# Kernel optimization log

Hardware: AMD Instinct MI355X
Metric: run time of the kernel (lower is better)

The kernel has to match this reference:

```python
import jax, jax.numpy as jnp
import numpy as np

B, N, D, F = 4096, 64, 64, 4096
KP_DIM = N * (N + 1) // 2  # 2080
# static row-major triu/tril index lists (matches torch.masked_select ordering)
_TRIU_I, _TRIU_J = (np.array(a) for a in np.triu_indices(N, 0))
_TRIL_I, _TRIL_J = (np.array(a) for a in np.tril_indices(N, 0))


def setup_inputs() -> dict:
    key = jax.random.key(0)
    k1, k2, k3, k4 = jax.random.split(key, 4)
    feature_emb = jax.random.normal(k1, (B, N, D), dtype=jnp.float32)
    # xavier_normal for [D, D]
    std = float(np.sqrt(2.0 / (D + D)))
    kp_W = jax.random.normal(k2, (D, D), dtype=jnp.float32) * std
    # nn.Linear weights are [out_features, in_features]
    bound = float(1.0 / np.sqrt(KP_DIM))
    W_triu = jax.random.uniform(k3, (F, KP_DIM), dtype=jnp.float32, minval=-bound, maxval=bound)
    W_tril = jax.random.uniform(k4, (F, KP_DIM), dtype=jnp.float32, minval=-bound, maxval=bound)
    return {"feature_emb": feature_emb, "kp_W": kp_W, "W_triu": W_triu, "W_tril": W_tril}


def reference(feature_emb, kp_W, W_triu, W_tril):
    # embs_kp[b,i,j] = e[b,i,:] @ kp_W @ e[b,j,:]  -> [B, N, N]
    embs_kp = jnp.einsum("bnd,de,bme->bnm", feature_emb, kp_W, feature_emb)
    triu = embs_kp[:, _TRIU_I, _TRIU_J]  # [B, kp_dim], row-major order
    tril = embs_kp[:, _TRIL_I, _TRIL_J]  # [B, kp_dim]
    embs_flatten = feature_emb.reshape(feature_emb.shape[0], -1)  # [B, N*D]
    view_1 = triu @ W_triu.T  # [B, F]
    view_2 = tril @ W_tril.T  # [B, F]
    return (embs_flatten, view_1, view_2)
```

## Files before the change

kernel.cpp:

```cpp
#include <hip/hip_runtime.h>

typedef __bf16 bf16x8 __attribute__((ext_vector_type(8)));
typedef float f32x4 __attribute__((ext_vector_type(4)));
typedef unsigned short u16x4 __attribute__((ext_vector_type(4)));
typedef unsigned short u16x8 __attribute__((ext_vector_type(8)));

#define KP 2112
#define NT 33

__device__ __forceinline__ unsigned short f2bf(float f) {
  unsigned int u = __builtin_bit_cast(unsigned int, f);
  u += 0x7FFFu + ((u >> 16) & 1u);
  return (unsigned short)(u >> 16);
}

__device__ __forceinline__ bf16x8 ld_frag(const unsigned short* p) {
  return __builtin_bit_cast(bf16x8, *(const u16x8*)p);
}

#define MFMA16(a, b, c) __builtin_amdgcn_mfma_f32_16x16x32_bf16((a), (b), (c), 0, 0, 0)

__device__ __forceinline__ void cp16(const void* g, void* l) {
  __builtin_amdgcn_global_load_lds(
      (const __attribute__((address_space(1))) unsigned int*)g,
      (__attribute__((address_space(3))) unsigned int*)l, 16, 0, 0);
}

__device__ __forceinline__ void barrier_sync() {
  asm volatile("" ::: "memory");
  __builtin_amdgcn_s_barrier();
  __builtin_amdgcn_sched_barrier(0);
}

#define VMWAIT(N) asm volatile("s_waitcnt vmcnt(" #N ")" ::: "memory")

__global__ __launch_bounds__(256) void cvt_pad(const float* __restrict__ in,
                                               unsigned short* __restrict__ out) {
  const int total = 4096 * (KP / 4);
  int i = blockIdx.x * 256 + threadIdx.x;
  const int stride = gridDim.x * 256;
  for (; i < total; i += stride) {
    const int row = i / (KP / 4);
    const int c4 = i - row * (KP / 4);
    u16x4 o = {0, 0, 0, 0};
    if (c4 < 520) {
      float4 v = *(const float4*)(in + (size_t)row * 2080 + c4 * 4);
      o[0] = f2bf(v.x); o[1] = f2bf(v.y); o[2] = f2bf(v.z); o[3] = f2bf(v.w);
    }
    ((u16x4*)out)[i] = o;
  }
}

__global__ __launch_bounds__(256) void prep_wt(const float* __restrict__ W,
                                               unsigned short* __restrict__ Wt) {
  const int tid = threadIdx.x;
#pragma unroll
  for (int j = 0; j < 16; ++j) {
    const int o = tid * 16 + j;
    const int c = o >> 6, d = o & 63;
    Wt[o] = f2bf(W[d * 64 + c]);
  }
}

__global__ __launch_bounds__(256) void batch_kp(
    const float* __restrict__ E,
    const unsigned short* __restrict__ Wt,
    float* __restrict__ out0,
    unsigned short* __restrict__ triu,
    unsigned short* __restrict__ tril)
{
  __shared__ __align__(16) unsigned short sE[64 * 64];
  __shared__ __align__(16) unsigned short sWt[64 * 64];
  __shared__ __align__(16) unsigned short sT[64 * 64];

  const int b = blockIdx.x;
  const int tid = threadIdx.x;
  const float* Eb = E + (size_t)b * 4096;
  float* o0 = out0 + (size_t)b * 4096;

  cp16(Wt + tid * 8, sWt + tid * 8);
  cp16(Wt + 2048 + tid * 8, sWt + 2048 + tid * 8);

#pragma unroll
  for (int it = 0; it < 4; ++it) {
    const int flat = it * 1024 + tid * 4;
    float4 v = *(const float4*)(Eb + flat);
    *(float4*)(o0 + flat) = v;
    u16x4 e;
    e[0] = f2bf(v.x); e[1] = f2bf(v.y); e[2] = f2bf(v.z); e[3] = f2bf(v.w);
    *(u16x4*)(sE + flat) = e;
  }
  __syncthreads();

  const int lane = tid & 63, w = tid >> 6;
  const int fr = lane & 15;
  const int fk = (lane >> 4) << 3;
  const int qr = (lane >> 4) << 2;

#pragma unroll
  for (int ct = 0; ct < 4; ++ct) {
    f32x4 acc = {0.f, 0.f, 0.f, 0.f};
#pragma unroll
    for (int k2 = 0; k2 < 2; ++k2) {
      bf16x8 a = ld_frag(sE + (w * 16 + fr) * 64 + k2 * 32 + fk);
      bf16x8 bb = ld_frag(sWt + (ct * 16 + fr) * 64 + k2 * 32 + fk);
      acc = MFMA16(a, bb, acc);
    }
#pragma unroll
    for (int r = 0; r < 4; ++r)
      sT[(w * 16 + qr + r) * 64 + ct * 16 + fr] = f2bf(acc[r]);
  }
  __syncthreads();

  unsigned short* tu = triu + (size_t)b * KP;
  unsigned short* tl = tril + (size_t)b * KP;
  if (tid < 32) { tu[2080 + tid] = 0; tl[2080 + tid] = 0; }
#pragma unroll
  for (int ct = 0; ct < 4; ++ct) {
    f32x4 acc = {0.f, 0.f, 0.f, 0.f};
#pragma unroll
    for (int k2 = 0; k2 < 2; ++k2) {
      bf16x8 a = ld_frag(sT + (w * 16 + fr) * 64 + k2 * 32 + fk);
      bf16x8 bb = ld_frag(sE + (ct * 16 + fr) * 64 + k2 * 32 + fk);
      acc = MFMA16(a, bb, acc);
    }
#pragma unroll
    for (int r = 0; r < 4; ++r) {
      const int i = w * 16 + qr + r;
      const int j = ct * 16 + fr;
      const unsigned short v = f2bf(acc[r]);
      if (j >= i) tu[i * 64 - ((i * (i - 1)) >> 1) + (j - i)] = v;
      if (j <= i) tl[((i * (i + 1)) >> 1) + j] = v;
    }
  }
}

__global__ __launch_bounds__(512, 2) void gemm_views(
    const unsigned short* __restrict__ triu, const unsigned short* __restrict__ tril,
    const unsigned short* __restrict__ Wu, const unsigned short* __restrict__ Wl,
    float* __restrict__ dout)
{
  __shared__ __align__(16) unsigned short lds[65536];

  const int z = blockIdx.z;
  const unsigned short* Ag = z ? tril : triu;
  const unsigned short* Bg = z ? Wl : Wu;
  float* C = dout + (size_t)16777216 * (size_t)(1 + z);

  const int tid = threadIdx.x;
  const int lane = tid & 63, wv = tid >> 6;
  const int m0 = blockIdx.y << 8, n0 = blockIdx.x << 8;

  const int lr = lane >> 3;
  const int cuch = (lane & 7) ^ lr;
  const int rA = wv * 8 + lr;
  const int rB = (wv & 3) * 8 + (wv >> 2) * 64 + lr;
  const unsigned short* gA = Ag + (size_t)(m0 + rA) * KP + cuch * 8;
  const unsigned short* gB = Bg + (size_t)(n0 + rB) * KP + cuch * 8;
  const int dA = tid * 8;
  const int dB = (wv & 3) * 512 + (wv >> 2) * 4096 + lane * 8;

  const int fr = lane & 15, fq = lane >> 4;
  const int sx0 = ((fq ^ (fr & 7))) * 8;
  const int sx1 = (((4 + fq) ^ (fr & 7))) * 8;
  const int rowA0 = (wv >> 2) * 128 + fr;
  const int rowB0 = (wv & 3) * 64 + fr;

  f32x4 acc[8][4] = {};
  bf16x8 af0[4], af1[4], bh0[2], bh1[2];

#define STAGE_A(B_, KT, OFF) do { \
    cp16(gA + (size_t)(OFF) * KP + (KT) * 64, lds + (B_) * 32768 + (OFF) * 64 + dA); \
    cp16(gA + (size_t)((OFF) + 128) * KP + (KT) * 64, \
         lds + (B_) * 32768 + ((OFF) + 128) * 64 + dA); \
  } while (0)
#define STAGE_B(B_, KT, OFF) do { \
    cp16(gB + (size_t)(OFF) * KP + (KT) * 64, \
         lds + (B_) * 32768 + 16384 + (OFF) * 64 + dB); \
    cp16(gB + (size_t)((OFF) + 128) * KP + (KT) * 64, \
         lds + (B_) * 32768 + 16384 + ((OFF) + 128) * 64 + dB); \
  } while (0)

#define PHASE(B_, MH, NH, LA, LB, STAGE_STMT, WAIT_STMT) do { \
    if (LA) { \
      const unsigned short* pa = lds + (B_) * 32768 + ((rowA0 + (MH) * 64) << 6); \
      _Pragma("unroll") for (int mt = 0; mt < 4; ++mt) { \
        af0[mt] = ld_frag(pa + mt * 1024 + sx0); \
        af1[mt] = ld_frag(pa + mt * 1024 + sx1); } } \
    if (LB) { \
      const unsigned short* pb = lds + (B_) * 32768 + 16384 + ((rowB0 + (NH) * 32) << 6); \
      _Pragma("unroll") for (int nt = 0; nt < 2; ++nt) { \
        bh0[nt] = ld_frag(pb + nt * 1024 + sx0); \
        bh1[nt] = ld_frag(pb + nt * 1024 + sx1); } } \
    STAGE_STMT; \
    barrier_sync(); \
    __builtin_amdgcn_s_setprio(1); \
    _Pragma("unroll") for (int mt = 0; mt < 4; ++mt) \
    _Pragma("unroll") for (int nt = 0; nt < 2; ++nt) { \
      acc[(MH)*4+mt][(NH)*2+nt] = MFMA16(af0[mt], bh0[nt], acc[(MH)*4+mt][(NH)*2+nt]); \
      acc[(MH)*4+mt][(NH)*2+nt] = MFMA16(af1[mt], bh1[nt], acc[(MH)*4+mt][(NH)*2+nt]); } \
    __builtin_amdgcn_s_setprio(0); \
    WAIT_STMT; \
    barrier_sync(); \
  } while (0)

  STAGE_A(0, 0, 0);
  STAGE_B(0, 0, 0);
  STAGE_A(0, 0, 64);
  STAGE_B(0, 0, 32);
  VMWAIT(4);
  barrier_sync();

  for (int t = 0; t < NT - 1; ++t) {
    const int cb = t & 1, nb = cb ^ 1, nk = t + 1;
    PHASE(cb, 0, 0, 1, 1, STAGE_A(nb, nk, 0),  VMWAIT(4));
    PHASE(cb, 1, 0, 1, 0, STAGE_B(nb, nk, 0),  VMWAIT(4));
    PHASE(cb, 1, 1, 0, 1, STAGE_A(nb, nk, 64), (void)0);
    PHASE(cb, 0, 1, 1, 0, STAGE_B(nb, nk, 32), VMWAIT(4));
  }
  {
    const int cb = (NT - 1) & 1;
    PHASE(cb, 0, 0, 1, 1, (void)0, VMWAIT(2));
    PHASE(cb, 1, 0, 1, 0, (void)0, VMWAIT(0));
    PHASE(cb, 1, 1, 0, 1, (void)0, (void)0);
    PHASE(cb, 0, 1, 1, 0, (void)0, (void)0);
  }

  const int qr = fq << 2;
  const int crow = m0 + (wv >> 2) * 128 + qr;
  const int ccol = n0 + (wv & 3) * 64 + fr;
#pragma unroll
  for (int mt = 0; mt < 8; ++mt)
#pragma unroll
    for (int nt = 0; nt < 4; ++nt) {
      float* cp = C + (size_t)(crow + mt * 16) * 4096 + (ccol + nt * 16);
#pragma unroll
      for (int r = 0; r < 4; ++r) cp[(size_t)r * 4096] = acc[mt][nt][r];
    }
#undef STAGE_A
#undef STAGE_B
#undef PHASE
}

extern "C" void kernel_launch(void* const* d_in, const int* in_sizes, int n_in,
                              void* d_out, int out_size, void* d_ws, size_t ws_size,
                              hipStream_t stream) {
  const float* feat  = (const float*)d_in[0];
  const float* kpW   = (const float*)d_in[1];
  const float* Wtriu = (const float*)d_in[2];
  const float* Wtril = (const float*)d_in[3];
  float* out = (float*)d_out;

  const size_t per = (size_t)4096 * KP;
  unsigned short* triu_bf = (unsigned short*)d_ws;
  unsigned short* tril_bf = triu_bf + per;
  unsigned short* Wu_bf   = tril_bf + per;
  unsigned short* Wl_bf   = Wu_bf + per;
  unsigned short* Wt_bf   = Wl_bf + per;

  cvt_pad<<<dim3(1024), dim3(256), 0, stream>>>(Wtriu, Wu_bf);
  cvt_pad<<<dim3(1024), dim3(256), 0, stream>>>(Wtril, Wl_bf);
  prep_wt<<<dim3(1), dim3(256), 0, stream>>>(kpW, Wt_bf);
  batch_kp<<<dim3(4096), dim3(256), 0, stream>>>(feat, Wt_bf, out, triu_bf, tril_bf);
  gemm_views<<<dim3(16, 16, 2), dim3(512), 0, stream>>>(triu_bf, tril_bf, Wu_bf, Wl_bf, out);
}
```

Before: 429.1 us.

## Restructure GEMM main loop into k-half phases with deeper prefetch schedule

Reorganizes the bf16 MFMA GEMM main loop so each phase covers one K-half with four N-tiles, rather than two K-halves with two N-tiles. LDS fragment loads for the next phase are issued before the current MFMAs, and global-to-LDS staging now runs up to two k-tiles ahead, overwriting regions of the current buffer once they are consumed. The aim is better overlap of LDS reads and global loads with MFMA work. In exchange it uses more fragment registers, and its hand-counted vmcnt waits, barrier placement and buffer reuse are fragile enough to risk races.

```diff
diff --git a/kernel.cpp b/kernel.cpp
--- a/kernel.cpp
+++ b/kernel.cpp
@@ -161,13 +161,11 @@
   const int dB = (wv & 3) * 512 + (wv >> 2) * 4096 + lane * 8;
 
   const int fr = lane & 15, fq = lane >> 4;
-  const int sx0 = ((fq ^ (fr & 7))) * 8;
-  const int sx1 = (((4 + fq) ^ (fr & 7))) * 8;
   const int rowA0 = (wv >> 2) * 128 + fr;
   const int rowB0 = (wv & 3) * 64 + fr;
 
   f32x4 acc[8][4] = {};
-  bf16x8 af0[4], af1[4], bh0[2], bh1[2];
+  bf16x8 aA_[4], aB_[4], bA_[4], bB_[4];
 
 #define STAGE_A(B_, KT, OFF) do { \
     cp16(gA + (size_t)(OFF) * KP + (KT) * 64, lds + (B_) * 32768 + (OFF) * 64 + dA); \
@@ -180,50 +178,64 @@
     cp16(gB + (size_t)((OFF) + 128) * KP + (KT) * 64, \
          lds + (B_) * 32768 + 16384 + ((OFF) + 128) * 64 + dB); \
   } while (0)
-
-#define PHASE(B_, MH, NH, LA, LB, STAGE_STMT, WAIT_STMT) do { \
-    if (LA) { \
-      const unsigned short* pa = lds + (B_) * 32768 + ((rowA0 + (MH) * 64) << 6); \
-      _Pragma("unroll") for (int mt = 0; mt < 4; ++mt) { \
-        af0[mt] = ld_frag(pa + mt * 1024 + sx0); \
-        af1[mt] = ld_frag(pa + mt * 1024 + sx1); } } \
-    if (LB) { \
-      const unsigned short* pb = lds + (B_) * 32768 + 16384 + ((rowB0 + (NH) * 32) << 6); \
-      _Pragma("unroll") for (int nt = 0; nt < 2; ++nt) { \
-        bh0[nt] = ld_frag(pb + nt * 1024 + sx0); \
-        bh1[nt] = ld_frag(pb + nt * 1024 + sx1); } } \
-    STAGE_STMT; \
-    barrier_sync(); \
+#define LDA(S, B_, MH, KH) do { _Pragma("unroll") \
+    for (int mt = 0; mt < 4; ++mt) \
+      S[mt] = ld_frag(lds + (B_) * 32768 + (rowA0 + (MH) * 64 + mt * 16) * 64 + \
+                      ((((KH) * 4 + fq) ^ (fr & 7)) * 8)); \
+  } while (0)
+#define LDB(S, B_, KH) do { _Pragma("unroll") \
+    for (int nt = 0; nt < 4; ++nt) \
+      S[nt] = ld_frag(lds + (B_) * 32768 + 16384 + (rowB0 + nt * 16) * 64 + \
+                      ((((KH) * 4 + fq) ^ (fr & 7)) * 8)); \
+  } while (0)
+#define PH_MFMA(AS, BS, MH) do { \
     __builtin_amdgcn_s_setprio(1); \
     _Pragma("unroll") for (int mt = 0; mt < 4; ++mt) \
-    _Pragma("unroll") for (int nt = 0; nt < 2; ++nt) { \
-      acc[(MH)*4+mt][(NH)*2+nt] = MFMA16(af0[mt], bh0[nt], acc[(MH)*4+mt][(NH)*2+nt]); \
-      acc[(MH)*4+mt][(NH)*2+nt] = MFMA16(af1[mt], bh1[nt], acc[(MH)*4+mt][(NH)*2+nt]); } \
+    _Pragma("unroll") for (int nt = 0; nt < 4; ++nt) \
+      acc[(MH) * 4 + mt][nt] = MFMA16(AS[mt], BS[nt], acc[(MH) * 4 + mt][nt]); \
     __builtin_amdgcn_s_setprio(0); \
-    WAIT_STMT; \
-    barrier_sync(); \
   } while (0)
 
   STAGE_A(0, 0, 0);
   STAGE_B(0, 0, 0);
+  STAGE_B(0, 0, 32);
   STAGE_A(0, 0, 64);
-  STAGE_B(0, 0, 32);
-  VMWAIT(4);
+  STAGE_B(1, 1, 0);
+  STAGE_B(1, 1, 32);
+  STAGE_A(1, 1, 0);
+  VMWAIT(6);
   barrier_sync();
-
-  for (int t = 0; t < NT - 1; ++t) {
-    const int cb = t & 1, nb = cb ^ 1, nk = t + 1;
-    PHASE(cb, 0, 0, 1, 1, STAGE_A(nb, nk, 0),  VMWAIT(4));
-    PHASE(cb, 1, 0, 1, 0, STAGE_B(nb, nk, 0),  VMWAIT(4));
-    PHASE(cb, 1, 1, 0, 1, STAGE_A(nb, nk, 64), (void)0);
-    PHASE(cb, 0, 1, 1, 0, STAGE_B(nb, nk, 32), VMWAIT(4));
-  }
-  {
-    const int cb = (NT - 1) & 1;
-    PHASE(cb, 0, 0, 1, 1, (void)0, VMWAIT(2));
-    PHASE(cb, 1, 0, 1, 0, (void)0, VMWAIT(0));
-    PHASE(cb, 1, 1, 0, 1, (void)0, (void)0);
-    PHASE(cb, 0, 1, 1, 0, (void)0, (void)0);
+  LDA(aB_, 0, 0, 0);
+  LDB(bA_, 0, 0);
+
+  for (int t = 0; t < NT; ++t) {
+    const int cb = t & 1, nb = cb ^ 1;
+    const int t1 = (t + 1 < NT) ? t + 1 : NT - 1;
+    const int t2 = (t + 2 < NT) ? t + 2 : NT - 1;
+    LDA(aA_, cb, 1, 0);
+    STAGE_A(nb, t1, 64);
+    barrier_sync();
+    PH_MFMA(aB_, bA_, 0);
+    barrier_sync();
+    LDA(aB_, cb, 1, 1);
+    LDB(bB_, cb, 1);
+    barrier_sync();
+    PH_MFMA(aA_, bA_, 1);
+    barrier_sync();
+    LDA(aA_, cb, 0, 1);
+    STAGE_B(cb, t2, 0);
+    barrier_sync();
+    PH_MFMA(aB_, bB_, 1);
+    VMWAIT(4);
+    barrier_sync();
+    LDA(aB_, nb, 0, 0);
+    LDB(bA_, nb, 0);
+    STAGE_B(cb, t2, 32);
+    STAGE_A(cb, t2, 0);
+    barrier_sync();
+    PH_MFMA(aA_, bB_, 0);
+    VMWAIT(6);
+    barrier_sync();
   }
 
   const int qr = fq << 2;
@@ -239,7 +251,9 @@
     }
 #undef STAGE_A
 #undef STAGE_B
-#undef PHASE
+#undef LDA
+#undef LDB
+#undef PH_MFMA
 }
 
 extern "C" void kernel_launch(void* const* d_in, const int* in_sizes, int n_in,
```

Result: no change. 426.5 us (-0.6%).
